# Performance work log

Measured on AMD Instinct MI355X. Metric: run time of the kernel, lower is better.

## Reference

```python
import jax, jax.numpy as jnp
import numpy as np

B, T, C = 128, 64, 66
S, L, W = 512, 2, 32  # state_size, num_layers, window_size


def _gru_cell(x, h, Wih, Whh, bih, bhh):
    # PyTorch GRU cell. x:[B,in], h:[B,S]; gate order r,z,n.
    gi = x @ Wih.T + bih  # [B,3S]
    gh = h @ Whh.T + bhh
    ir, iz, inn = jnp.split(gi, 3, axis=-1)
    hr, hz, hn = jnp.split(gh, 3, axis=-1)
    r = jax.nn.sigmoid(ir + hr)
    z = jax.nn.sigmoid(iz + hz)
    n = jnp.tanh(inn + r * hn)
    return (1.0 - z) * n + z * h


def setup_inputs() -> dict:
    key = jax.random.key(0)
    ks = jax.random.split(key, 14)
    sc = 0.02
    inp = {
        'x': jax.random.normal(ks[0], (B, T, C), dtype=jnp.float32),
        'Wih0': jax.random.normal(ks[1], (3 * S, C), dtype=jnp.float32) * sc,
        'Whh0': jax.random.normal(ks[2], (3 * S, S), dtype=jnp.float32) * sc,
        'bih0': jax.random.normal(ks[3], (3 * S,), dtype=jnp.float32) * sc,
        'bhh0': jax.random.normal(ks[4], (3 * S,), dtype=jnp.float32) * sc,
        'Wih1': jax.random.normal(ks[5], (3 * S, S), dtype=jnp.float32) * sc,
        'Whh1': jax.random.normal(ks[6], (3 * S, S), dtype=jnp.float32) * sc,
        'bih1': jax.random.normal(ks[7], (3 * S,), dtype=jnp.float32) * sc,
        'bhh1': jax.random.normal(ks[8], (3 * S,), dtype=jnp.float32) * sc,
        'Wt': jax.random.normal(ks[9], (1, W), dtype=jnp.float32) * sc,   # temporal_fc_last: Linear(W,1)
        'bt': jnp.zeros((1,), dtype=jnp.float32),
        'Ws': jax.random.normal(ks[10], (C, S), dtype=jnp.float32) * sc,  # spatial_fc: Linear(S,C)
        'bs': jnp.zeros((C,), dtype=jnp.float32),
    }
    return inp


def reference(x, Wih0, Whh0, bih0, bhh0, Wih1, Whh1, bih1, bhh1, Wt, bt, Ws, bs):
    Bx, Tx, Cx = x.shape
    h0 = jnp.zeros((Bx, S), dtype=x.dtype)
    h1 = jnp.zeros((Bx, S), dtype=x.dtype)

    def stack_step(h0, h1, xt):
        h0 = _gru_cell(xt, h0, Wih0, Whh0, bih0, bhh0)
        h1 = _gru_cell(h0, h1, Wih1, Whh1, bih1, bhh1)
        return h0, h1

    # ---- encoder over x[:, :-1, :] ----
    def enc_step(carry, xt):
        h0, h1 = stack_step(carry[0], carry[1], xt)
        return (h0, h1), h1

    (h0, h1), enc_out = jax.lax.scan(enc_step, (h0, h1), x[:, :-1, :].transpose(1, 0, 2))
    # enc_out: [T-1, B, S]; sliding window of the last W encoder outputs: [B, W, S]
    window = enc_out[-W:].transpose(1, 0, 2)

    def dec_step(carry, _):
        h0, h1, win, dinp = carry  # dinp: [B, C]
        h0, h1 = stack_step(h0, h1, dinp)
        win = jnp.concatenate([win[:, 1:, :], h1[:, None, :]], axis=1)  # slide window
        # temporal_fc_last over time axis (after b n d -> b d n): [B, S]
        temp = jnp.einsum('bws,w->bs', win, Wt[0]) + bt[0]
        out = temp @ Ws.T + bs  # spatial_fc: [B, C]
        new_frame = out + dinp  # recursive residual
        return (h0, h1, win, new_frame), new_frame

    init = (h0, h1, window, x[:, -1, :])
    _, frames = jax.lax.scan(dec_step, init, None, length=Tx)  # [T, B, C]
    return frames.transpose(1, 0, 2)  # [B, T, C]
```

## Files before the change

### kernel.cpp

```cpp
#include <hip/hip_runtime.h>
#include <stdint.h>

typedef unsigned short u16;
typedef uint32_t u32;
typedef __attribute__((ext_vector_type(8))) short short8;
typedef __attribute__((ext_vector_type(4))) float floatx4;
typedef __attribute__((ext_vector_type(2))) unsigned int u32x2;

constexpr int BB = 128;
constexpr int TT = 64;
constexpr int CC = 66;
constexpr int CPAD = 96;
constexpr int SS = 512;
constexpr int NGATE = 1536;
constexpr int NGRP = 8;
constexpr int GBLK = 16;
constexpr int GS = 16 * SS;


__device__ __forceinline__ u16 f2bf(float f) {
    u32 u = __float_as_uint(f);
    u32 r = (u + 0x7fffu + ((u >> 16) & 1u)) >> 16;
    return (u16)r;
}
__device__ __forceinline__ float bf2f(u16 h) {
    return __uint_as_float(((u32)h) << 16);
}
__device__ __forceinline__ float sigm(float x) { return 1.f / (1.f + __expf(-x)); }
__device__ __forceinline__ float tanh_f(float x) { return 1.f - 2.f / (1.f + __expf(2.f * x)); }

__device__ __forceinline__ void load_issue_cc(const u16* p, short8& d) {
    asm volatile("global_load_dwordx4 %0, %1, off sc0 sc1"
                 : "=v"(d) : "v"(p));
}
__device__ __forceinline__ void store_u64_cc(u16* p, u32x2 v) {
    asm volatile("global_store_dwordx2 %0, %1, off sc0 sc1"
                 :: "v"(p), "v"(v) : "memory");
}
__device__ __forceinline__ void vm_drain() {
    asm volatile("s_waitcnt vmcnt(0)" ::: "memory");
}

__global__ void prep1_kernel(const float* __restrict__ x,
                             const float* __restrict__ Wih0,
                             const float* __restrict__ Whh0,
                             const float* __restrict__ Wih1,
                             const float* __restrict__ Whh1,
                             const float* __restrict__ Ws,
                             u16* __restrict__ xbf, u16* __restrict__ wi0,
                             u16* __restrict__ wh0, u16* __restrict__ wi1,
                             u16* __restrict__ wh1, u16* __restrict__ wsb)
{
    const int N_xbf = BB * TT * CPAD;
    const int N_wi0 = NGATE * CPAD;
    const int N_whh = NGATE * SS;
    const int N_wsb = 80 * SS;
    const long total = (long)N_xbf + N_wi0 + 3L * N_whh + N_wsb;
    for (long i = (long)blockIdx.x * blockDim.x + threadIdx.x; i < total;
         i += (long)gridDim.x * blockDim.x) {
        long idx = i;
        if (idx < N_xbf) {
            int c = idx % CPAD; int bt = idx / CPAD;
            float v = (c < CC) ? x[(long)bt * CC + c] : 0.f;
            xbf[idx] = f2bf(v); continue;
        }
        idx -= N_xbf;
        if (idx < N_wi0) {
            int c = idx % CPAD; int n = idx / CPAD;
            float v = (c < CC) ? Wih0[(long)n * CC + c] : 0.f;
            wi0[idx] = f2bf(v); continue;
        }
        idx -= N_wi0;
        if (idx < N_whh) { wh0[idx] = f2bf(Whh0[idx]); continue; }
        idx -= N_whh;
        if (idx < N_whh) { wi1[idx] = f2bf(Wih1[idx]); continue; }
        idx -= N_whh;
        if (idx < N_whh) { wh1[idx] = f2bf(Whh1[idx]); continue; }
        idx -= N_whh;
        {
            int s = idx % SS; int c = idx / SS;
            wsb[idx] = (c < CC) ? f2bf(Ws[(long)c * SS + s]) : (u16)0;
        }
    }
}

__global__ void prep2_kernel(const float* __restrict__ x,
                             const float* __restrict__ Wih0,
                             const float* __restrict__ Ws,
                             const float* __restrict__ bs,
                             u16* __restrict__ Mbf, float* __restrict__ c0vec,
                             float* __restrict__ gi0i)
{
    const long NM = (long)NGATE * SS;
    const long NC = NGATE;
    const long NG = (long)BB * NGATE;
    const long total = NM + NC + NG;
    for (long i = (long)blockIdx.x * blockDim.x + threadIdx.x; i < total;
         i += (long)gridDim.x * blockDim.x) {
        long idx = i;
        if (idx < NM) {
            int s = idx % SS; int g = idx / SS;
            float acc = 0.f;
            for (int c = 0; c < CC; ++c)
                acc += Wih0[(long)g * CC + c] * Ws[(long)c * SS + s];
            Mbf[idx] = f2bf(acc); continue;
        }
        idx -= NM;
        if (idx < NC) {
            int g = idx;
            float acc = 0.f;
            for (int c = 0; c < CC; ++c) acc += Wih0[(long)g * CC + c] * bs[c];
            c0vec[g] = acc; continue;
        }
        idx -= NC;
        {
            int g = idx % NGATE; int b = idx / NGATE;
            float acc = 0.f;
            const float* xl = x + ((long)b * TT + (TT - 1)) * CC;
            for (int c = 0; c < CC; ++c) acc += xl[c] * Wih0[(long)g * CC + c];
            gi0i[idx] = acc;
        }
    }
}

__device__ __forceinline__ void load_afrags(const u16* __restrict__ st,
                                            int lane, short8* a) {
#pragma unroll
    for (int kc = 0; kc < 16; ++kc)
        load_issue_cc(st + (long)kc * 512 + lane * 8, a[kc]);
}

#define MFMA_BF16(a, wp, acc) \
    acc = __builtin_amdgcn_mfma_f32_16x16x32_bf16(a, *(const short8*)(wp), acc, 0, 0, 0)

__device__ __forceinline__ void mm3_reg(const short8* a,
                                        const u16* __restrict__ w0,
                                        const u16* __restrict__ w1,
                                        const u16* __restrict__ w2,
                                        floatx4& A0, floatx4& A1, floatx4& A2) {
#pragma unroll
    for (int kc = 0; kc < 16; ++kc) {
        const int k = kc << 5;
        MFMA_BF16(a[kc], w0 + k, A0);
        MFMA_BF16(a[kc], w1 + k, A1);
        MFMA_BF16(a[kc], w2 + k, A2);
    }
}

template <int K>
__device__ __forceinline__ void mm3_g(const u16* __restrict__ aP,
                                      const u16* __restrict__ w0,
                                      const u16* __restrict__ w1,
                                      const u16* __restrict__ w2,
                                      floatx4& A0, floatx4& A1, floatx4& A2) {
#pragma unroll
    for (int k = 0; k < K; k += 32) {
        short8 a = *(const short8*)(aP + k);
        MFMA_BF16(a, w0 + k, A0);
        MFMA_BF16(a, w1 + k, A1);
        MFMA_BF16(a, w2 + k, A2);
    }
}

__device__ __forceinline__ void waitc2(const int* __restrict__ c0, int s0,
                                       const int* __restrict__ c1, int s1) {
    const int lane = threadIdx.x & 63;
    const int* p = (lane < 32) ? (c0 + s0) : (c1 + s1);
    const bool act = ((lane < 32) ? s0 : s1) > 0;
    for (;;) {
        int v = 32;
        if (act)
            v = __hip_atomic_load(p, __ATOMIC_RELAXED, __HIP_MEMORY_SCOPE_AGENT);
        if (__all(v >= 32)) break;
        __builtin_amdgcn_s_sleep(2);
    }
    asm volatile("" ::: "memory");
}

__device__ __forceinline__ void waitc1(const int* __restrict__ c, int s) {
    const int* p = c + s;
    for (;;) {
        int v = __hip_atomic_load(p, __ATOMIC_RELAXED, __HIP_MEMORY_SCOPE_AGENT);
        if (__all(v >= 32)) break;
        __builtin_amdgcn_s_sleep(2);
    }
    asm volatile("" ::: "memory");
}

__device__ __forceinline__ void bump(int* c, int s) {
    if ((threadIdx.x & 63) == 0)
        __hip_atomic_fetch_add(c + s, 1, __ATOMIC_RELAXED,
                               __HIP_MEMORY_SCOPE_AGENT);
}

__device__ __forceinline__ void staged_store(u16* __restrict__ gdst,
                                             u16* __restrict__ lds,
                                             const u16 hb[4],
                                             int l15, int quad, int lane)
{
#pragma unroll
    for (int r = 0; r < 4; ++r)
        lds[((l15 >> 3) << 7) + ((quad << 2) + r) * 8 + (l15 & 7)] = hb[r];
    __builtin_amdgcn_wave_barrier();
    const u32* lp = (const u32*)(lds + (lane << 2));
    u32x2 v; v[0] = lp[0]; v[1] = lp[1];
    store_u64_cc(gdst + (lane << 2), v);
    __builtin_amdgcn_wave_barrier();
}

__global__ __launch_bounds__(256, 1) void persist_kernel(
    const u16* __restrict__ xbf,
    const u16* __restrict__ wi0, const u16* __restrict__ wh0,
    const u16* __restrict__ wi1, const u16* __restrict__ wh1,
    const u16* __restrict__ Mbf,
    const float* __restrict__ bih0, const float* __restrict__ bhh0,
    const float* __restrict__ bih1, const float* __restrict__ bhh1,
    const float* __restrict__ c0vec, const float* __restrict__ gi0i,
    const float* __restrict__ Wt, const float* __restrict__ bt,
    u16* __restrict__ h0buf,
    u16* __restrict__ h1buf,
    u16* __restrict__ tstage,
    u16* __restrict__ temps,
    int* __restrict__ gcnt)
{
    const int tid = threadIdx.x;
    const int wave = tid >> 6, lane = tid & 63;
    const int l15 = lane & 15, quad = lane >> 4;
    const int grp = blockIdx.x >> 4, rank = blockIdx.x & 15;
    const int b0g = grp * 16;
    const int wsub = wave & 1;
    const int sg = rank * 32 + wsub * 16 + l15;
    const bool l0w = wave < 2;

    __shared__ u16 stg[4][512];
    u16* const ldsH = &stg[wave][0];
    u16* const ldsT = &stg[wave][256];

    const int wbase = (rank * 4 + wsub * 2) << 7;

    u16* const h0g = h0buf + (long)grp * 4 * GS;
    u16* const h1g = h1buf + (long)grp * 2 * GS;
    u16* const tsg = tstage + (long)grp * 2 * GS;
    int* const c0 = gcnt + grp * 256;
    int* const c1 = c0 + 128;

    float bir, biz, bin, bhn;
    float c0r = 0.f, c0z = 0.f, c0n = 0.f;
    float hf[4] = {0.f, 0.f, 0.f, 0.f};
    float gi[12];
    float wt[32]; float btv = 0.f;
    u32 wreg[4][16];
#pragma unroll
    for (int r = 0; r < 4; ++r)
#pragma unroll
        for (int i = 0; i < 16; ++i) wreg[r][i] = 0u;

    if (l0w) {
        bir = bih0[sg] + bhh0[sg];
        biz = bih0[512 + sg] + bhh0[512 + sg];
        bin = bih0[1024 + sg];
        bhn = bhh0[1024 + sg];
        c0r = c0vec[sg]; c0z = c0vec[512 + sg]; c0n = c0vec[1024 + sg];
#pragma unroll
        for (int g3 = 0; g3 < 3; ++g3)
#pragma unroll
            for (int r = 0; r < 4; ++r)
                gi[g3 * 4 + r] =
                    gi0i[(long)(b0g + quad * 4 + r) * NGATE + g3 * 512 + sg];
    } else {
        bir = bih1[sg] + bhh1[sg];
        biz = bih1[512 + sg] + bhh1[512 + sg];
        bin = bih1[1024 + sg];
        bhn = bhh1[1024 + sg];
#pragma unroll
        for (int j = 0; j < 32; ++j) wt[j] = Wt[j];
        btv = bt[0];
    }

    const u16 *wiR, *wiZ, *wiN, *whR, *whZ, *whN, *mR, *mZ, *mN;
    if (l0w) {
        wiR = wi0 + (long)sg * CPAD + quad * 8;
        wiZ = wi0 + (long)(512 + sg) * CPAD + quad * 8;
        wiN = wi0 + (long)(1024 + sg) * CPAD + quad * 8;
        whR = wh0 + (long)sg * SS + quad * 8;
        whZ = wh0 + (long)(512 + sg) * SS + quad * 8;
        whN = wh0 + (long)(1024 + sg) * SS + quad * 8;
        mR = Mbf + (long)sg * SS + quad * 8;
        mZ = Mbf + (long)(512 + sg) * SS + quad * 8;
        mN = Mbf + (long)(1024 + sg) * SS + quad * 8;
    } else {
        wiR = wi1 + (long)sg * SS + quad * 8;
        wiZ = wi1 + (long)(512 + sg) * SS + quad * 8;
        wiN = wi1 + (long)(1024 + sg) * SS + quad * 8;
        whR = wh1 + (long)sg * SS + quad * 8;
        whZ = wh1 + (long)(512 + sg) * SS + quad * 8;
        whN = wh1 + (long)(1024 + sg) * SS + quad * 8;
        mR = mZ = mN = nullptr;
    }

    short8 fa[16], fb[16];

    if (l0w) {
        for (int t = 0; t < 63; ++t) {
            waitc2(c0, t, c1, t - 3);
            load_afrags(h0g + (long)(t & 3) * GS, lane, fa);
            floatx4 aR = {0,0,0,0}, aZ = aR, aNI = aR, aNH = aR;
            const u16* aP = xbf + ((long)(b0g + l15) * TT + t) * CPAD + quad * 8;
            mm3_g<CPAD>(aP, wiR, wiZ, wiN, aR, aZ, aNI);
            vm_drain();
            mm3_reg(fa, whR, whZ, whN, aR, aZ, aNH);
            u16 hb[4];
#pragma unroll
            for (int r = 0; r < 4; ++r) {
                float rr = sigm(aR[r] + bir);
                float zz = sigm(aZ[r] + biz);
                float nn = tanh_f(aNI[r] + bin + rr * (aNH[r] + bhn));
                float hv = (1.f - zz) * nn + zz * hf[r];
                hf[r] = hv;
                hb[r] = f2bf(hv);
            }
            staged_store(h0g + (long)((t + 1) & 3) * GS + wbase, ldsH, hb,
                         l15, quad, lane);
            vm_drain();
            bump(c0, t + 1);
        }
        for (int d = 0; d < 64; ++d) {
            const int t = 63 + d;
            waitc2(c0, t, c1, t - 3);
            load_afrags(h0g + (long)(t & 3) * GS, lane, fa);
            vm_drain();
            floatx4 hR = {0,0,0,0}, hZ = hR, hN4 = hR;
            mm3_reg(fa, whR, whZ, whN, hR, hZ, hN4);
            if (d > 0) {
                waitc1(c1, t);
                load_afrags(tsg + (long)((d - 1) & 1) * GS, lane, fb);
                vm_drain();
                floatx4 tR = {0,0,0,0}, tZ = tR, tN = tR;
                mm3_reg(fb, mR, mZ, mN, tR, tZ, tN);
#pragma unroll
                for (int r = 0; r < 4; ++r) {
                    gi[r] += tR[r] + c0r;
                    gi[4 + r] += tZ[r] + c0z;
                    gi[8 + r] += tN[r] + c0n;
                }
            }
            u16 hb[4];
#pragma unroll
            for (int r = 0; r < 4; ++r) {
                float rr = sigm(gi[r] + hR[r] + bir);
                float zz = sigm(gi[4 + r] + hZ[r] + biz);
                float nn = tanh_f(gi[8 + r] + bin + rr * (hN4[r] + bhn));
                float hv = (1.f - zz) * nn + zz * hf[r];
                hf[r] = hv;
                hb[r] = f2bf(hv);
            }
            staged_store(h0g + (long)((t + 1) & 3) * GS + wbase, ldsH, hb,
                         l15, quad, lane);
            vm_drain();
            bump(c0, t + 1);
        }
    } else {
        for (int u = 0; u < 63; ++u) {
            if (u > 0) {
                waitc1(c1, u);
            }
            load_afrags(h1g + (long)(u & 1) * GS, lane, fb);
            vm_drain();
            floatx4 aR = {0,0,0,0}, aZ = aR, aNI = aR, aNH = aR;
            mm3_reg(fb, whR, whZ, whN, aR, aZ, aNH);
            waitc1(c0, u + 1);
            load_afrags(h0g + (long)((u + 1) & 3) * GS, lane, fa);
            vm_drain();
            mm3_reg(fa, wiR, wiZ, wiN, aR, aZ, aNI);
            u16 hb[4];
#pragma unroll
            for (int r = 0; r < 4; ++r) {
                float rr = sigm(aR[r] + bir);
                float zz = sigm(aZ[r] + biz);
                float nn = tanh_f(aNI[r] + bin + rr * (aNH[r] + bhn));
                float hv = (1.f - zz) * nn + zz * hf[r];
                hf[r] = hv;
                u16 v = f2bf(hv);
                hb[r] = v;
#pragma unroll
                for (int i = 0; i < 15; ++i)
                    wreg[r][i] = (wreg[r][i] >> 16) | (wreg[r][i + 1] << 16);
                wreg[r][15] = (wreg[r][15] >> 16) | ((u32)v << 16);
            }
            staged_store(h1g + (long)((u + 1) & 1) * GS + wbase, ldsH, hb,
                         l15, quad, lane);
            vm_drain();
            bump(c1, u + 1);
        }
        for (int d = 0; d < 64; ++d) {
            const int u = 63 + d;
            waitc1(c1, u);
            load_afrags(h1g + (long)(u & 1) * GS, lane, fb);
            vm_drain();
            floatx4 aR = {0,0,0,0}, aZ = aR, aNI = aR, aNH = aR;
            mm3_reg(fb, whR, whZ, whN, aR, aZ, aNH);
            waitc1(c0, u + 1);
            load_afrags(h0g + (long)((u + 1) & 3) * GS, lane, fa);
            vm_drain();
            mm3_reg(fa, wiR, wiZ, wiN, aR, aZ, aNI);
            u16* tOut = temps + (long)d * (BB * SS);
            u16 hb[4], tb4[4];
#pragma unroll
            for (int r = 0; r < 4; ++r) {
                float rr = sigm(aR[r] + bir);
                float zz = sigm(aZ[r] + biz);
                float nn = tanh_f(aNI[r] + bin + rr * (aNH[r] + bhn));
                float hv = (1.f - zz) * nn + zz * hf[r];
                hf[r] = hv;
                u16 v = f2bf(hv);
                hb[r] = v;
#pragma unroll
                for (int i = 0; i < 15; ++i)
                    wreg[r][i] = (wreg[r][i] >> 16) | (wreg[r][i + 1] << 16);
                wreg[r][15] = (wreg[r][15] >> 16) | ((u32)v << 16);
                float tacc = btv;
#pragma unroll
                for (int i = 0; i < 16; ++i) {
                    u32 wv = wreg[r][i];
                    tacc += __uint_as_float(wv << 16) * wt[2 * i];
                    tacc += __uint_as_float(wv & 0xffff0000u) * wt[2 * i + 1];
                }
                u16 tb = f2bf(tacc);
                tb4[r] = tb;
                tOut[(long)(b0g + quad * 4 + r) * SS + sg] = tb;
            }
            staged_store(h1g + (long)((u + 1) & 1) * GS + wbase, ldsH, hb,
                         l15, quad, lane);
            staged_store(tsg + (long)(d & 1) * GS + wbase, ldsT, tb4,
                         l15, quad, lane);
            vm_drain();
            bump(c1, u + 1);
        }
    }
}

__global__ __launch_bounds__(256) void frames_kernel(
    const u16* __restrict__ temps, const float* __restrict__ x,
    const u16* __restrict__ wsb, const float* __restrict__ bs,
    float* __restrict__ outp)
{
    const int b = blockIdx.x, tid = threadIdx.x;
    const int wave = tid >> 6, lane = tid & 63;
    const int l15 = lane & 15, quad = lane >> 4;
    __shared__ float P[64][81];

    const int e0 = wave * 16;
    floatx4 acc[5];
#pragma unroll
    for (int ct = 0; ct < 5; ++ct) acc[ct] = (floatx4){0.f, 0.f, 0.f, 0.f};
    const u16* aBase =
        temps + (long)(e0 + l15) * (BB * SS) + (long)b * SS + quad * 8;
#pragma unroll
    for (int kc = 0; kc < 16; ++kc) {
        short8 a = *(const short8*)(aBase + kc * 32);
#pragma unroll
        for (int ct = 0; ct < 5; ++ct) {
            const u16* wp = wsb + (long)(ct * 16 + l15) * SS + quad * 8 + kc * 32;
            MFMA_BF16(a, wp, acc[ct]);
        }
    }
#pragma unroll
    for (int ct = 0; ct < 5; ++ct)
#pragma unroll
        for (int r = 0; r < 4; ++r)
            P[e0 + quad * 4 + r][ct * 16 + l15] = acc[ct][r];
    __syncthreads();

    const int c = tid;
    if (c < CC) {
        float cum = x[((long)b * TT + (TT - 1)) * CC + c];
        const float bsv = bs[c];
        for (int e = 0; e < TT; ++e) {
            cum += P[e][c] + bsv;
            outp[(long)b * TT * CC + (long)e * CC + c] = cum;
        }
    }
}

extern "C" void kernel_launch(void* const* d_in, const int* in_sizes, int n_in,
                              void* d_out, int out_size, void* d_ws, size_t ws_size,
                              hipStream_t stream)
{
    const float* x    = (const float*)d_in[0];
    const float* Wih0 = (const float*)d_in[1];
    const float* Whh0 = (const float*)d_in[2];
    const float* bih0 = (const float*)d_in[3];
    const float* bhh0 = (const float*)d_in[4];
    const float* Wih1 = (const float*)d_in[5];
    const float* Whh1 = (const float*)d_in[6];
    const float* bih1 = (const float*)d_in[7];
    const float* bhh1 = (const float*)d_in[8];
    const float* Wt   = (const float*)d_in[9];
    const float* bt   = (const float*)d_in[10];
    const float* Ws   = (const float*)d_in[11];
    const float* bs   = (const float*)d_in[12];
    float* outp = (float*)d_out;

    char* p = (char*)d_ws;
    auto alloc = [&](size_t bytes) -> char* {
        char* r = p; p += (bytes + 255) & ~(size_t)255; return r;
    };
    u16* h0buf = (u16*)alloc((size_t)NGRP * 4 * GS * 2);
    u16* h1buf = (u16*)alloc((size_t)NGRP * 2 * GS * 2);
    u16* tstage = (u16*)alloc((size_t)NGRP * 2 * GS * 2);
    u16* xbf = (u16*)alloc((size_t)BB * TT * CPAD * 2);
    u16* wi0 = (u16*)alloc((size_t)NGATE * CPAD * 2);
    u16* wh0 = (u16*)alloc((size_t)NGATE * SS * 2);
    u16* wi1 = (u16*)alloc((size_t)NGATE * SS * 2);
    u16* wh1 = (u16*)alloc((size_t)NGATE * SS * 2);
    u16* Mbf = (u16*)alloc((size_t)NGATE * SS * 2);
    u16* wsb = (u16*)alloc((size_t)80 * SS * 2);
    float* c0vec = (float*)alloc((size_t)NGATE * 4);
    float* gi0i  = (float*)alloc((size_t)BB * NGATE * 4);
    u16* temps = (u16*)alloc((size_t)TT * BB * SS * 2);
    int* gcnt = (int*)alloc((size_t)NGRP * 256 * 4);

    hipMemsetAsync(h0buf, 0, (size_t)NGRP * 4 * GS * 2, stream);
    hipMemsetAsync(h1buf, 0, (size_t)NGRP * 2 * GS * 2, stream);
    hipMemsetAsync(gcnt, 0, (size_t)NGRP * 256 * 4, stream);

    prep1_kernel<<<1024, 256, 0, stream>>>(x, Wih0, Whh0, Wih1, Whh1, Ws,
                                           xbf, wi0, wh0, wi1, wh1, wsb);
    prep2_kernel<<<1024, 256, 0, stream>>>(x, Wih0, Ws, bs, Mbf, c0vec, gi0i);

    persist_kernel<<<NGRP * GBLK, 256, 0, stream>>>(
        xbf, wi0, wh0, wi1, wh1, Mbf, bih0, bhh0, bih1, bhh1,
        c0vec, gi0i, Wt, bt, h0buf, h1buf, tstage, temps, gcnt);

    frames_kernel<<<BB, 256, 0, stream>>>(temps, x, wsb, bs, outp);
}
```

Baseline: 2.423 ms.

## Probe XCD co-location at runtime and use L2-coherent loads within group

Remaps blocks so that each 16-block group is formed from blockIdx values congruent mod 8, which likely places the whole group on one XCD. At startup a handshake checks whether the blocks can see each other's stores through sc0-only (L2-scoped) accesses. If every block in the group agrees, the kernel runs a templated body that uses sc0 loads and stores instead of sc0 sc1, which avoids going past L2 for the hidden-state exchange. Otherwise it falls back to the old coherent path. This relies on the dispatch-to-XCD mapping, and the heuristic probe could accept a case where sc0-only visibility is not actually guaranteed.

```diff
diff --git a/kernel.cpp b/kernel.cpp
--- a/kernel.cpp
+++ b/kernel.cpp
@@ -29,16 +29,34 @@
 __device__ __forceinline__ float sigm(float x) { return 1.f / (1.f + __expf(-x)); }
 __device__ __forceinline__ float tanh_f(float x) { return 1.f - 2.f / (1.f + __expf(2.f * x)); }
 
+template <bool XL>
 __device__ __forceinline__ void load_issue_cc(const u16* p, short8& d) {
-    asm volatile("global_load_dwordx4 %0, %1, off sc0 sc1"
-                 : "=v"(d) : "v"(p));
-}
+    if constexpr (XL)
+        asm volatile("global_load_dwordx4 %0, %1, off sc0" : "=v"(d) : "v"(p));
+    else
+        asm volatile("global_load_dwordx4 %0, %1, off sc0 sc1" : "=v"(d) : "v"(p));
+}
+template <bool XL>
 __device__ __forceinline__ void store_u64_cc(u16* p, u32x2 v) {
-    asm volatile("global_store_dwordx2 %0, %1, off sc0 sc1"
-                 :: "v"(p), "v"(v) : "memory");
+    if constexpr (XL)
+        asm volatile("global_store_dwordx2 %0, %1, off sc0"
+                     :: "v"(p), "v"(v) : "memory");
+    else
+        asm volatile("global_store_dwordx2 %0, %1, off sc0 sc1"
+                     :: "v"(p), "v"(v) : "memory");
 }
 __device__ __forceinline__ void vm_drain() {
     asm volatile("s_waitcnt vmcnt(0)" ::: "memory");
+}
+
+__device__ __forceinline__ int ld_sc0(const int* p) {
+    int v;
+    asm volatile("global_load_dword %0, %1, off sc0\n\ts_waitcnt vmcnt(0)"
+                 : "=&v"(v) : "v"(p) : "memory");
+    return v;
+}
+__device__ __forceinline__ void st_sc0(int* p, int v) {
+    asm volatile("global_store_dword %0, %1, off sc0" :: "v"(p), "v"(v) : "memory");
 }
 
 __global__ void prep1_kernel(const float* __restrict__ x,
@@ -123,11 +141,12 @@
     }
 }
 
+template <bool XL>
 __device__ __forceinline__ void load_afrags(const u16* __restrict__ st,
                                             int lane, short8* a) {
 #pragma unroll
     for (int kc = 0; kc < 16; ++kc)
-        load_issue_cc(st + (long)kc * 512 + lane * 8, a[kc]);
+        load_issue_cc<XL>(st + (long)kc * 512 + lane * 8, a[kc]);
 }
 
 #define MFMA_BF16(a, wp, acc) \
@@ -193,6 +212,7 @@
                                __HIP_MEMORY_SCOPE_AGENT);
 }
 
+template <bool XL>
 __device__ __forceinline__ void staged_store(u16* __restrict__ gdst,
                                              u16* __restrict__ lds,
                                              const u16 hb[4],
@@ -204,11 +224,13 @@
     __builtin_amdgcn_wave_barrier();
     const u32* lp = (const u32*)(lds + (lane << 2));
     u32x2 v; v[0] = lp[0]; v[1] = lp[1];
-    store_u64_cc(gdst + (lane << 2), v);
+    store_u64_cc<XL>(gdst + (lane << 2), v);
     __builtin_amdgcn_wave_barrier();
 }
 
-__global__ __launch_bounds__(256, 1) void persist_kernel(
+template <bool XL>
+__device__ __forceinline__ void persist_body(
+    const int grp, const int rank,
     const u16* __restrict__ xbf,
     const u16* __restrict__ wi0, const u16* __restrict__ wh0,
     const u16* __restrict__ wi1, const u16* __restrict__ wh1,
@@ -217,24 +239,20 @@
     const float* __restrict__ bih1, const float* __restrict__ bhh1,
     const float* __restrict__ c0vec, const float* __restrict__ gi0i,
     const float* __restrict__ Wt, const float* __restrict__ bt,
-    u16* __restrict__ h0buf,
-    u16* __restrict__ h1buf,
-    u16* __restrict__ tstage,
-    u16* __restrict__ temps,
-    int* __restrict__ gcnt)
+    u16* __restrict__ h0buf, u16* __restrict__ h1buf,
+    u16* __restrict__ tstage, u16* __restrict__ temps,
+    int* __restrict__ gcnt, u16* __restrict__ stgBase)
 {
     const int tid = threadIdx.x;
     const int wave = tid >> 6, lane = tid & 63;
     const int l15 = lane & 15, quad = lane >> 4;
-    const int grp = blockIdx.x >> 4, rank = blockIdx.x & 15;
     const int b0g = grp * 16;
     const int wsub = wave & 1;
     const int sg = rank * 32 + wsub * 16 + l15;
     const bool l0w = wave < 2;
 
-    __shared__ u16 stg[4][512];
-    u16* const ldsH = &stg[wave][0];
-    u16* const ldsT = &stg[wave][256];
+    u16* const ldsH = stgBase + wave * 512;
+    u16* const ldsT = ldsH + 256;
 
     const int wbase = (rank * 4 + wsub * 2) << 7;
 
@@ -303,7 +321,7 @@
     if (l0w) {
         for (int t = 0; t < 63; ++t) {
             waitc2(c0, t, c1, t - 3);
-            load_afrags(h0g + (long)(t & 3) * GS, lane, fa);
+            load_afrags<XL>(h0g + (long)(t & 3) * GS, lane, fa);
             floatx4 aR = {0,0,0,0}, aZ = aR, aNI = aR, aNH = aR;
             const u16* aP = xbf + ((long)(b0g + l15) * TT + t) * CPAD + quad * 8;
             mm3_g<CPAD>(aP, wiR, wiZ, wiN, aR, aZ, aNI);
@@ -319,21 +337,21 @@
                 hf[r] = hv;
                 hb[r] = f2bf(hv);
             }
-            staged_store(h0g + (long)((t + 1) & 3) * GS + wbase, ldsH, hb,
-                         l15, quad, lane);
+            staged_store<XL>(h0g + (long)((t + 1) & 3) * GS + wbase, ldsH, hb,
+                             l15, quad, lane);
             vm_drain();
             bump(c0, t + 1);
         }
         for (int d = 0; d < 64; ++d) {
             const int t = 63 + d;
             waitc2(c0, t, c1, t - 3);
-            load_afrags(h0g + (long)(t & 3) * GS, lane, fa);
+            load_afrags<XL>(h0g + (long)(t & 3) * GS, lane, fa);
             vm_drain();
             floatx4 hR = {0,0,0,0}, hZ = hR, hN4 = hR;
             mm3_reg(fa, whR, whZ, whN, hR, hZ, hN4);
             if (d > 0) {
                 waitc1(c1, t);
-                load_afrags(tsg + (long)((d - 1) & 1) * GS, lane, fb);
+                load_afrags<XL>(tsg + (long)((d - 1) & 1) * GS, lane, fb);
                 vm_drain();
                 floatx4 tR = {0,0,0,0}, tZ = tR, tN = tR;
                 mm3_reg(fb, mR, mZ, mN, tR, tZ, tN);
@@ -354,8 +372,8 @@
                 hf[r] = hv;
                 hb[r] = f2bf(hv);
             }
-            staged_store(h0g + (long)((t + 1) & 3) * GS + wbase, ldsH, hb,
-                         l15, quad, lane);
+            staged_store<XL>(h0g + (long)((t + 1) & 3) * GS + wbase, ldsH, hb,
+                             l15, quad, lane);
             vm_drain();
             bump(c0, t + 1);
         }
@@ -364,12 +382,12 @@
             if (u > 0) {
                 waitc1(c1, u);
             }
-            load_afrags(h1g + (long)(u & 1) * GS, lane, fb);
+            load_afrags<XL>(h1g + (long)(u & 1) * GS, lane, fb);
             vm_drain();
             floatx4 aR = {0,0,0,0}, aZ = aR, aNI = aR, aNH = aR;
             mm3_reg(fb, whR, whZ, whN, aR, aZ, aNH);
             waitc1(c0, u + 1);
-            load_afrags(h0g + (long)((u + 1) & 3) * GS, lane, fa);
+            load_afrags<XL>(h0g + (long)((u + 1) & 3) * GS, lane, fa);
             vm_drain();
             mm3_reg(fa, wiR, wiZ, wiN, aR, aZ, aNI);
             u16 hb[4];
@@ -387,20 +405,20 @@
                     wreg[r][i] = (wreg[r][i] >> 16) | (wreg[r][i + 1] << 16);
                 wreg[r][15] = (wreg[r][15] >> 16) | ((u32)v << 16);
             }
-            staged_store(h1g + (long)((u + 1) & 1) * GS + wbase, ldsH, hb,
-                         l15, quad, lane);
+            staged_store<XL>(h1g + (long)((u + 1) & 1) * GS + wbase, ldsH, hb,
+                             l15, quad, lane);
             vm_drain();
             bump(c1, u + 1);
         }
         for (int d = 0; d < 64; ++d) {
             const int u = 63 + d;
             waitc1(c1, u);
-            load_afrags(h1g + (long)(u & 1) * GS, lane, fb);
+            load_afrags<XL>(h1g + (long)(u & 1) * GS, lane, fb);
             vm_drain();
             floatx4 aR = {0,0,0,0}, aZ = aR, aNI = aR, aNH = aR;
             mm3_reg(fb, whR, whZ, whN, aR, aZ, aNH);
             waitc1(c0, u + 1);
-            load_afrags(h0g + (long)((u + 1) & 3) * GS, lane, fa);
+            load_afrags<XL>(h0g + (long)((u + 1) & 3) * GS, lane, fa);
             vm_drain();
             mm3_reg(fa, wiR, wiZ, wiN, aR, aZ, aNI);
             u16* tOut = temps + (long)d * (BB * SS);
@@ -429,13 +447,73 @@
                 tb4[r] = tb;
                 tOut[(long)(b0g + quad * 4 + r) * SS + sg] = tb;
             }
-            staged_store(h1g + (long)((u + 1) & 1) * GS + wbase, ldsH, hb,
-                         l15, quad, lane);
-            staged_store(tsg + (long)(d & 1) * GS + wbase, ldsT, tb4,
-                         l15, quad, lane);
+            staged_store<XL>(h1g + (long)((u + 1) & 1) * GS + wbase, ldsH, hb,
+                             l15, quad, lane);
+            staged_store<XL>(tsg + (long)(d & 1) * GS + wbase, ldsT, tb4,
+                             l15, quad, lane);
             vm_drain();
             bump(c1, u + 1);
         }
+    }
+}
+
+__global__ __launch_bounds__(256, 1) void persist_kernel(
+    const u16* __restrict__ xbf,
+    const u16* __restrict__ wi0, const u16* __restrict__ wh0,
+    const u16* __restrict__ wi1, const u16* __restrict__ wh1,
+    const u16* __restrict__ Mbf,
+    const float* __restrict__ bih0, const float* __restrict__ bhh0,
+    const float* __restrict__ bih1, const float* __restrict__ bhh1,
+    const float* __restrict__ c0vec, const float* __restrict__ gi0i,
+    const float* __restrict__ Wt, const float* __restrict__ bt,
+    u16* __restrict__ h0buf, u16* __restrict__ h1buf,
+    u16* __restrict__ tstage, u16* __restrict__ temps,
+    int* __restrict__ gcnt)
+{
+    const int grp = blockIdx.x & 7;
+    const int rank = blockIdx.x >> 3;
+    __shared__ u16 stg[4 * 512];
+    __shared__ int smode;
+
+    if (threadIdx.x == 0) {
+        int* meta = gcnt + NGRP * 256;
+        int* hs = meta + grp * 256;
+        int* votes = meta + 2048;
+        int* arr = meta + 2056;
+        int ok = 1;
+        for (int gen = 1; gen <= 3 && ok; ++gen) {
+            st_sc0(hs + rank * 16, gen);
+            vm_drain();
+            int iters = 0;
+            for (;;) {
+                int good = 1;
+                for (int r = 0; r < GBLK; ++r)
+                    if (ld_sc0(hs + r * 16) < gen) { good = 0; break; }
+                if (good) break;
+                if (++iters > 1024) { ok = 0; break; }
+                __builtin_amdgcn_s_sleep(2);
+            }
+        }
+        __hip_atomic_fetch_add(votes + grp, ok, __ATOMIC_RELAXED,
+                               __HIP_MEMORY_SCOPE_AGENT);
+        __hip_atomic_fetch_add(arr + grp, 1, __ATOMIC_RELEASE,
+                               __HIP_MEMORY_SCOPE_AGENT);
+        while (__hip_atomic_load(arr + grp, __ATOMIC_ACQUIRE,
+                                 __HIP_MEMORY_SCOPE_AGENT) < GBLK)
+            __builtin_amdgcn_s_sleep(2);
+        smode = (__hip_atomic_load(votes + grp, __ATOMIC_RELAXED,
+                                   __HIP_MEMORY_SCOPE_AGENT) == GBLK) ? 1 : 0;
+    }
+    __syncthreads();
+
+    if (smode) {
+        persist_body<true>(grp, rank, xbf, wi0, wh0, wi1, wh1, Mbf,
+                           bih0, bhh0, bih1, bhh1, c0vec, gi0i, Wt, bt,
+                           h0buf, h1buf, tstage, temps, gcnt, stg);
+    } else {
+        persist_body<false>(grp, rank, xbf, wi0, wh0, wi1, wh1, Mbf,
+                            bih0, bhh0, bih1, bhh1, c0vec, gi0i, Wt, bt,
+                            h0buf, h1buf, tstage, temps, gcnt, stg);
     }
 }
 
@@ -518,11 +596,11 @@
     float* c0vec = (float*)alloc((size_t)NGATE * 4);
     float* gi0i  = (float*)alloc((size_t)BB * NGATE * 4);
     u16* temps = (u16*)alloc((size_t)TT * BB * SS * 2);
-    int* gcnt = (int*)alloc((size_t)NGRP * 256 * 4);
+    int* gcnt = (int*)alloc((size_t)(NGRP * 256 + 2048 + 16) * 4);
 
     hipMemsetAsync(h0buf, 0, (size_t)NGRP * 4 * GS * 2, stream);
     hipMemsetAsync(h1buf, 0, (size_t)NGRP * 2 * GS * 2, stream);
-    hipMemsetAsync(gcnt, 0, (size_t)NGRP * 256 * 4, stream);
+    hipMemsetAsync(gcnt, 0, (size_t)(NGRP * 256 + 2048 + 16) * 4, stream);
 
     prep1_kernel<<<1024, 256, 0, stream>>>(x, Wih0, Whh0, Wih1, Whh1, Ws,
                                            xbf, wi0, wh0, wi1, wh1, wsb);
```

Result: slower. 2.922 ms (+20.6%).
